# Optimization experiments

Measured on AMD Instinct MI355X. Metric: run time of the kernel, lower is better.

Reference implementation:

```python
import jax, jax.numpy as jnp
import numpy as np

B, N, F_IN = 16, 2048, 64   # batch, node_num, input_dim
D = 64                      # dim == embed_dim == GNN out_channel
TOPK = 30
EPS = 1e-5
NEG_SLOPE = 0.2


def setup_inputs() -> dict:
    key = jax.random.key(0)
    k = jax.random.split(key, 20)
    u = lambda kk, shp, b: jax.random.uniform(kk, shp, jnp.float32, -b, b)
    return {
        "data": jax.random.normal(k[0], (B, N, F_IN), jnp.float32),
        "org_edge_index": jax.random.randint(k[1], (2, N * TOPK), 0, N),  # accepted but unused (prior_graph=True)
        "embedding_weight": u(k[2], (N, D), 1.0 / np.sqrt(D)),            # kaiming_uniform(a=sqrt(5)) bound
        "lin_w": u(k[3], (F_IN, D), 1.0 / np.sqrt(F_IN)),
        "att_i": jax.random.normal(k[4], (D,), jnp.float32) * 0.1,
        "att_j": jax.random.normal(k[5], (D,), jnp.float32) * 0.1,
        "att_em_i": jax.random.normal(k[6], (D,), jnp.float32) * 0.1,
        "att_em_j": jax.random.normal(k[7], (D,), jnp.float32) * 0.1,
        "gnn_bias": jax.random.normal(k[8], (D,), jnp.float32) * 0.01,
        "bn1_gamma": jax.random.uniform(k[9], (D,), jnp.float32, 0.5, 1.5),
        "bn1_beta": jax.random.normal(k[10], (D,), jnp.float32) * 0.1,
        "bn1_mean": jax.random.normal(k[11], (D,), jnp.float32) * 0.1,
        "bn1_var": jax.random.uniform(k[12], (D,), jnp.float32, 0.5, 1.5),
        "bn2_gamma": jax.random.uniform(k[13], (D,), jnp.float32, 0.5, 1.5),
        "bn2_beta": jax.random.normal(k[14], (D,), jnp.float32) * 0.1,
        "bn2_mean": jax.random.normal(k[15], (D,), jnp.float32) * 0.1,
        "bn2_var": jax.random.uniform(k[16], (D,), jnp.float32, 0.5, 1.5),
        "out_w": u(k[17], (D, 1), 1.0 / np.sqrt(D)),
        "out_b": jnp.zeros((1,), jnp.float32),
    }


def _forward(data, org_edge_index, embedding_weight, lin_w, att_i, att_j,
             att_em_i, att_em_j, gnn_bias,
             bn1_gamma, bn1_beta, bn1_mean, bn1_var,
             bn2_gamma, bn2_beta, bn2_mean, bn2_var,
             out_w, out_b):
    b, n, f = data.shape
    x = jax.lax.stop_gradient(data).reshape(b * n, f)  # torch: x = data.clone().detach()

    # --- dynamic graph: top-k cosine similarity over DETACHED embeddings ---
    w = jax.lax.stop_gradient(embedding_weight)        # weights_arr = embedding.detach().clone()
    nrm = jnp.linalg.norm(w, axis=-1, keepdims=True)
    cos = (w @ w.T) / (nrm * nrm.T)                    # [N, N]
    _, topk_idx = jax.lax.top_k(cos, TOPK)             # [N, k]; row i contains i itself (cos(i,i)=1 is the max),
                                                       # so remove_self_loops + add_self_loops leaves the edge set unchanged
    # batched sources; target of edge (i, kk) is node i -> each node receives exactly TOPK edges
    src = (topk_idx[None] + (jnp.arange(b) * n)[:, None, None]).reshape(b * n, TOPK)

    # --- GraphLayer (GAT-style, heads=1, concat=False -> mean over 1 head) ---
    xl = x @ lin_w                                     # [BN, D]
    emb_all = jnp.tile(embedding_weight, (b, 1))       # [BN, D] embeddings repeated per batch
    a_i = xl @ att_i + emb_all @ att_em_i              # per-node target score [BN]
    a_j = xl @ att_j + emb_all @ att_em_j              # per-node source score [BN]
    alpha = jax.nn.leaky_relu(a_i[:, None] + a_j[src], NEG_SLOPE)  # [BN, k]
    alpha = jax.nn.softmax(alpha, axis=-1)             # softmax over incoming edges per target node
    out = jnp.einsum('ek,ekd->ed', alpha, xl[src]) + gnn_bias      # per-edge gather + weighted add-aggregate

    # GNNLayer: BatchNorm1d (eval) + ReLU
    out = (out - bn1_mean) / jnp.sqrt(bn1_var + EPS) * bn1_gamma + bn1_beta
    out = jax.nn.relu(out)

    # --- readout ---
    h = out.reshape(b, n, D) * embedding_weight[None]  # elementwise mul with node embeddings
    h = (h - bn2_mean) / jnp.sqrt(bn2_var + EPS) * bn2_gamma + bn2_beta  # bn_outlayer_in (eval)
    h = jax.nn.relu(h)                                 # dropout = identity (eval)
    y = h @ out_w + out_b                              # OutLayer: single Linear(D, 1)
    return y.reshape(-1, n)                            # [B, N]


def reference(data, org_edge_index, embedding_weight, lin_w, att_i, att_j,
              att_em_i, att_em_j, gnn_bias,
              bn1_gamma, bn1_beta, bn1_mean, bn1_var,
              bn2_gamma, bn2_beta, bn2_mean, bn2_var,
              out_w, out_b):
    return _forward(data, org_edge_index, embedding_weight, lin_w, att_i, att_j,
                    att_em_i, att_em_j, gnn_bias,
                    bn1_gamma, bn1_beta, bn1_mean, bn1_var,
                    bn2_gamma, bn2_beta, bn2_mean, bn2_var,
                    out_w, out_b)
```

## Files before the change

### kernel.cpp

```cpp
#include <hip/hip_runtime.h>
#include <hip/hip_bf16.h>

#define NODES 2048
#define DIM   64
#define K_TOP 30
#define BATCH 16
#define BN    (NODES * BATCH)
#define NEGINF (-3.402823466e38f)
#define EPS 1e-5f
#define TB 64

template <int CTRL>
__device__ __forceinline__ float dpp_add_f32(float x) {
    int y = __builtin_amdgcn_update_dpp(0, __float_as_int(x), CTRL, 0xf, 0xf, true);
    return x + __int_as_float(y);
}

__device__ __forceinline__ float wave_sum(float x) {
    x = dpp_add_f32<0x111>(x);
    x = dpp_add_f32<0x112>(x);
    x = dpp_add_f32<0x114>(x);
    x = dpp_add_f32<0x118>(x);
    x = dpp_add_f32<0x142>(x);
    x = dpp_add_f32<0x143>(x);
    return __int_as_float(__builtin_amdgcn_readlane(__float_as_int(x), 63));
}

template <int CTRL>
__device__ __forceinline__ float dpp_max_f32(float x) {
    int y = __builtin_amdgcn_update_dpp(__float_as_int(x), __float_as_int(x),
                                        CTRL, 0xf, 0xf, false);
    return fmaxf(x, __int_as_float(y));
}

__device__ __forceinline__ float wave_max(float x) {
    x = dpp_max_f32<0x111>(x);
    x = dpp_max_f32<0x112>(x);
    x = dpp_max_f32<0x114>(x);
    x = dpp_max_f32<0x118>(x);
    x = dpp_max_f32<0x142>(x);
    x = dpp_max_f32<0x143>(x);
    return __int_as_float(__builtin_amdgcn_readlane(__float_as_int(x), 63));
}

#define ARGMAX_STEP(CTRL)                                                       \
    do {                                                                        \
        int nv_ = __builtin_amdgcn_update_dpp(__float_as_int(bv),               \
                      __float_as_int(bv), (CTRL), 0xf, 0xf, false);             \
        int nj_ = __builtin_amdgcn_update_dpp(bj, bj, (CTRL), 0xf, 0xf, false); \
        float nvf_ = __int_as_float(nv_);                                       \
        bool g_ = (nvf_ > bv) || (nvf_ == bv && nj_ < bj);                      \
        bv = g_ ? nvf_ : bv;                                                    \
        bj = g_ ? nj_ : bj;                                                     \
    } while (0)

__global__ __launch_bounds__(256) void normalize_kernel(const float* __restrict__ w,
                                                        float* __restrict__ wn) {
    int r = blockIdx.x * 4 + (threadIdx.x >> 6);
    int lane = threadIdx.x & 63;
    float v = w[r * DIM + lane];
    float s = wave_sum(v * v);
    wn[r * DIM + lane] = v * rsqrtf(s);
}

__global__ __launch_bounds__(256) void cos_kernel(const float* __restrict__ wn,
                                                  float* __restrict__ cosm) {
    __shared__ float As[TB][DIM + 1];
    __shared__ float Bs[TB][DIM + 1];
    const int tid = threadIdx.x;
    const int bi = blockIdx.x, bj = blockIdx.y;

    for (int s = tid; s < TB * DIM; s += 256) {
        int r = s >> 6, d = s & 63;
        As[r][d] = wn[(bi * TB + r) * DIM + d];
        Bs[r][d] = wn[(bj * TB + r) * DIM + d];
    }
    __syncthreads();

    const int ti = tid >> 4, tj = tid & 15;
    float acc[4][4] = {};
    #pragma unroll 16
    for (int k = 0; k < DIM; ++k) {
        float a[4], b[4];
        #pragma unroll
        for (int u = 0; u < 4; ++u) a[u] = As[ti * 4 + u][k];
        #pragma unroll
        for (int v = 0; v < 4; ++v) b[v] = Bs[tj * 4 + v][k];
        #pragma unroll
        for (int u = 0; u < 4; ++u)
            #pragma unroll
            for (int v = 0; v < 4; ++v)
                acc[u][v] = fmaf(a[u], b[v], acc[u][v]);
    }
    #pragma unroll
    for (int u = 0; u < 4; ++u) {
        float4 o = make_float4(acc[u][0], acc[u][1], acc[u][2], acc[u][3]);
        *(float4*)&cosm[(size_t)(bi * TB + ti * 4 + u) * NODES + bj * TB + tj * 4] = o;
    }
}

__global__ __launch_bounds__(256) void topk_kernel(const float* __restrict__ cosm,
                                                   int* __restrict__ topk) {
    const int i = blockIdx.x * 4 + (threadIdx.x >> 6);
    const int lane = threadIdx.x & 63;
    const float* row = cosm + (size_t)i * NODES;

    float v[NODES / 64];
    #pragma unroll
    for (int q = 0; q < NODES / 64; ++q) v[q] = row[q * 64 + lane];

    int res = 0;
    for (int t = 0; t < K_TOP; ++t) {
        float lm = v[0];
        int lq = 0;
        #pragma unroll
        for (int q = 1; q < NODES / 64; ++q) {
            bool g = v[q] > lm;
            lm = g ? v[q] : lm;
            lq = g ? q : lq;
        }
        float bv = lm;
        int bj = lq * 64 + lane;
        ARGMAX_STEP(0x111);
        ARGMAX_STEP(0x112);
        ARGMAX_STEP(0x114);
        ARGMAX_STEP(0x118);
        ARGMAX_STEP(0x142);
        ARGMAX_STEP(0x143);
        const int wj = __builtin_amdgcn_readlane(bj, 63);
        res = (lane == t) ? wj : res;
        const int wl = wj & 63;
        const int wq = wj >> 6;
        #pragma unroll
        for (int q = 0; q < NODES / 64; ++q)
            if (q == wq && lane == wl) v[q] = NEGINF;
    }
    if (lane < K_TOP) topk[i * K_TOP + lane] = res;
}

__global__ __launch_bounds__(256) void lin_kernel(const float* __restrict__ x,
                                                  const float* __restrict__ lin_w,
                                                  const float* __restrict__ emb,
                                                  const float* __restrict__ att_i,
                                                  const float* __restrict__ att_j,
                                                  const float* __restrict__ att_em_i,
                                                  const float* __restrict__ att_em_j,
                                                  float* __restrict__ xl,
                                                  float* __restrict__ ai,
                                                  float* __restrict__ aj) {
    __shared__ float lw[DIM * DIM];
    __shared__ float xs[16 * DIM];
    const int tid = threadIdx.x;
    const int wave = tid >> 6;
    const int lane = tid & 63;
    const int row0 = blockIdx.x * 16;

    for (int t = tid; t < DIM * DIM; t += 256) lw[t] = lin_w[t];
    for (int t = tid; t < 16 * DIM; t += 256) xs[t] = x[row0 * DIM + t];
    __syncthreads();

    for (int rr = wave; rr < 16; rr += 4) {
        const int r = row0 + rr;
        float acc = 0.f;
        #pragma unroll
        for (int f = 0; f < DIM; ++f)
            acc = fmaf(xs[rr * DIM + f], lw[f * DIM + lane], acc);
        xl[r * DIM + lane] = acc;

        const int i = r & (NODES - 1);
        const float em = emb[i * DIM + lane];
        float ti = wave_sum(acc * att_i[lane] + em * att_em_i[lane]);
        float tj = wave_sum(acc * att_j[lane] + em * att_em_j[lane]);
        if (lane == 0) { ai[r] = ti; aj[r] = tj; }
    }
}

__global__ __launch_bounds__(256) void agg_kernel(const int* __restrict__ topk,
                                                  const float* __restrict__ xl,
                                                  const float* __restrict__ ai,
                                                  const float* __restrict__ aj,
                                                  const float* __restrict__ emb,
                                                  const float* __restrict__ gnn_bias,
                                                  const float* __restrict__ g1, const float* __restrict__ b1,
                                                  const float* __restrict__ m1, const float* __restrict__ v1,
                                                  const float* __restrict__ g2, const float* __restrict__ b2,
                                                  const float* __restrict__ m2, const float* __restrict__ v2,
                                                  const float* __restrict__ out_w,
                                                  const float* __restrict__ out_b,
                                                  float* __restrict__ y) {
    const int e = blockIdx.x * 4 + (threadIdx.x >> 6);
    const int lane = threadIdx.x & 63;
    const int i = e & (NODES - 1);
    const int b = e >> 11;

    const float a_ie = ai[e];
    int nbr = 0;
    float raw = NEGINF;
    if (lane < K_TOP) {
        nbr = (b << 11) + topk[i * K_TOP + lane];
        float r0 = a_ie + aj[nbr];
        raw = (r0 >= 0.f) ? r0 : 0.2f * r0;
    }
    const float m = wave_max(raw);
    float p = (lane < K_TOP) ? __expf(raw - m) : 0.f;
    const float s = wave_sum(p);
    const float inv = 1.f / s;

    float acc = 0.f;
    #pragma unroll
    for (int k = 0; k < K_TOP; ++k) {
        const float pk = __int_as_float(__builtin_amdgcn_readlane(__float_as_int(p), k));
        const int nb = __builtin_amdgcn_readlane(nbr, k);
        acc = fmaf(pk, xl[nb * DIM + lane], acc);
    }

    float o = acc * inv + gnn_bias[lane];
    o = (o - m1[lane]) * rsqrtf(v1[lane] + EPS) * g1[lane] + b1[lane];
    o = fmaxf(o, 0.f);
    float h = o * emb[i * DIM + lane];
    h = (h - m2[lane]) * rsqrtf(v2[lane] + EPS) * g2[lane] + b2[lane];
    h = fmaxf(h, 0.f);
    float t = wave_sum(h * out_w[lane]);
    if (lane == 0) y[e] = t + out_b[0];
}

extern "C" void kernel_launch(void* const* d_in, const int* in_sizes, int n_in,
                              void* d_out, int out_size, void* d_ws, size_t ws_size,
                              hipStream_t stream) {
    const float* data      = (const float*)d_in[0];
    const float* emb       = (const float*)d_in[2];
    const float* lin_w     = (const float*)d_in[3];
    const float* att_i     = (const float*)d_in[4];
    const float* att_j     = (const float*)d_in[5];
    const float* att_em_i  = (const float*)d_in[6];
    const float* att_em_j  = (const float*)d_in[7];
    const float* gnn_bias  = (const float*)d_in[8];
    const float* bn1_gamma = (const float*)d_in[9];
    const float* bn1_beta  = (const float*)d_in[10];
    const float* bn1_mean  = (const float*)d_in[11];
    const float* bn1_var   = (const float*)d_in[12];
    const float* bn2_gamma = (const float*)d_in[13];
    const float* bn2_beta  = (const float*)d_in[14];
    const float* bn2_mean  = (const float*)d_in[15];
    const float* bn2_var   = (const float*)d_in[16];
    const float* out_w     = (const float*)d_in[17];
    const float* out_b     = (const float*)d_in[18];
    float* y = (float*)d_out;

    char* ws = (char*)d_ws;
    float* cosm = (float*)(ws);
    float* xl   = (float*)(ws);
    float* ai   = (float*)(ws + 8 * 1024 * 1024);
    float* aj   = (float*)(ws + 8 * 1024 * 1024 + 131072);
    float* wn   = (float*)(ws + 16 * 1024 * 1024);
    int*   topk = (int*)  (ws + 16 * 1024 * 1024 + 524288);

    normalize_kernel<<<NODES / 4, 256, 0, stream>>>(emb, wn);
    cos_kernel<<<dim3(NODES / TB, NODES / TB), 256, 0, stream>>>(wn, cosm);
    topk_kernel<<<NODES / 4, 256, 0, stream>>>(cosm, topk);
    lin_kernel<<<BN / 16, 256, 0, stream>>>(data, lin_w, emb, att_i, att_j,
                                            att_em_i, att_em_j, xl, ai, aj);
    agg_kernel<<<BN / 4, 256, 0, stream>>>(topk, xl, ai, aj, emb, gnn_bias,
                                           bn1_gamma, bn1_beta, bn1_mean, bn1_var,
                                           bn2_gamma, bn2_beta, bn2_mean, bn2_var,
                                           out_w, out_b, y);
}
```

Baseline: 178.8 us.

## Retile cosine GEMM with transposed LDS and tree-reduce per-lane top-k argmax

The cosine-similarity kernel moves to 128x128 tiles with 512 threads, an 8x4 register tile per thread, and embeddings stored transposed in shared memory so each step reads operands as float4. This is meant to raise compute per shared-memory load and cut load instruction count, at the cost of more registers and possible bank conflicts on the transposed stores. The top-k kernel replaces the serial 32-element per-lane argmax chain with a pairwise tree reduction, which shortens the dependency chain in each of the 30 selection rounds. The tree keeps the lower index on ties, so results stay the same.

```diff
diff --git a/kernel.cpp b/kernel.cpp
--- a/kernel.cpp
+++ b/kernel.cpp
@@ -8,7 +8,8 @@
 #define BN    (NODES * BATCH)
 #define NEGINF (-3.402823466e38f)
 #define EPS 1e-5f
-#define TB 64
+#define TBC 128
+#define KPAD 132
 
 template <int CTRL>
 __device__ __forceinline__ float dpp_add_f32(float x) {
@@ -63,39 +64,42 @@
     wn[r * DIM + lane] = v * rsqrtf(s);
 }
 
-__global__ __launch_bounds__(256) void cos_kernel(const float* __restrict__ wn,
+__global__ __launch_bounds__(512) void cos_kernel(const float* __restrict__ wn,
                                                   float* __restrict__ cosm) {
-    __shared__ float As[TB][DIM + 1];
-    __shared__ float Bs[TB][DIM + 1];
+    __shared__ float AsT[DIM][KPAD];
+    __shared__ float BsT[DIM][KPAD];
     const int tid = threadIdx.x;
     const int bi = blockIdx.x, bj = blockIdx.y;
 
-    for (int s = tid; s < TB * DIM; s += 256) {
+    #pragma unroll
+    for (int it = 0; it < 16; ++it) {
+        int s = it * 512 + tid;
         int r = s >> 6, d = s & 63;
-        As[r][d] = wn[(bi * TB + r) * DIM + d];
-        Bs[r][d] = wn[(bj * TB + r) * DIM + d];
+        AsT[d][r] = wn[(bi * TBC + r) * DIM + d];
+        BsT[d][r] = wn[(bj * TBC + r) * DIM + d];
     }
     __syncthreads();
 
-    const int ti = tid >> 4, tj = tid & 15;
-    float acc[4][4] = {};
-    #pragma unroll 16
+    const int ti = tid >> 5;
+    const int tj = tid & 31;
+    float acc[8][4] = {};
+    #pragma unroll 4
     for (int k = 0; k < DIM; ++k) {
-        float a[4], b[4];
-        #pragma unroll
-        for (int u = 0; u < 4; ++u) a[u] = As[ti * 4 + u][k];
-        #pragma unroll
-        for (int v = 0; v < 4; ++v) b[v] = Bs[tj * 4 + v][k];
-        #pragma unroll
-        for (int u = 0; u < 4; ++u)
+        float4 a0 = *(const float4*)&AsT[k][ti * 8];
+        float4 a1 = *(const float4*)&AsT[k][ti * 8 + 4];
+        float4 b0 = *(const float4*)&BsT[k][tj * 4];
+        float a[8] = {a0.x, a0.y, a0.z, a0.w, a1.x, a1.y, a1.z, a1.w};
+        float b[4] = {b0.x, b0.y, b0.z, b0.w};
+        #pragma unroll
+        for (int u = 0; u < 8; ++u)
             #pragma unroll
             for (int v = 0; v < 4; ++v)
                 acc[u][v] = fmaf(a[u], b[v], acc[u][v]);
     }
     #pragma unroll
-    for (int u = 0; u < 4; ++u) {
+    for (int u = 0; u < 8; ++u) {
         float4 o = make_float4(acc[u][0], acc[u][1], acc[u][2], acc[u][3]);
-        *(float4*)&cosm[(size_t)(bi * TB + ti * 4 + u) * NODES + bj * TB + tj * 4] = o;
+        *(float4*)&cosm[(size_t)(bi * TBC + ti * 8 + u) * NODES + bj * TBC + tj * 4] = o;
     }
 }
 
@@ -111,16 +115,24 @@
 
     int res = 0;
     for (int t = 0; t < K_TOP; ++t) {
-        float lm = v[0];
-        int lq = 0;
-        #pragma unroll
-        for (int q = 1; q < NODES / 64; ++q) {
-            bool g = v[q] > lm;
-            lm = g ? v[q] : lm;
-            lq = g ? q : lq;
+        float tv[16]; int tq[16];
+        #pragma unroll
+        for (int u = 0; u < 16; ++u) {
+            bool g = v[2 * u + 1] > v[2 * u];
+            tv[u] = g ? v[2 * u + 1] : v[2 * u];
+            tq[u] = g ? (2 * u + 1) : (2 * u);
         }
-        float bv = lm;
-        int bj = lq * 64 + lane;
+        #pragma unroll
+        for (int h = 8; h >= 1; h >>= 1) {
+            #pragma unroll
+            for (int u = 0; u < h; ++u) {
+                bool g = tv[u + h] > tv[u];
+                tv[u] = g ? tv[u + h] : tv[u];
+                tq[u] = g ? tq[u + h] : tq[u];
+            }
+        }
+        float bv = tv[0];
+        int bj = tq[0] * 64 + lane;
         ARGMAX_STEP(0x111);
         ARGMAX_STEP(0x112);
         ARGMAX_STEP(0x114);
@@ -256,7 +268,7 @@
     int*   topk = (int*)  (ws + 16 * 1024 * 1024 + 524288);
 
     normalize_kernel<<<NODES / 4, 256, 0, stream>>>(emb, wn);
-    cos_kernel<<<dim3(NODES / TB, NODES / TB), 256, 0, stream>>>(wn, cosm);
+    cos_kernel<<<dim3(NODES / TBC, NODES / TBC), 512, 0, stream>>>(wn, cosm);
     topk_kernel<<<NODES / 4, 256, 0, stream>>>(cosm, topk);
     lin_kernel<<<BN / 16, 256, 0, stream>>>(data, lin_w, emb, att_i, att_j,
                                             att_em_i, att_em_j, xl, ai, aj);
```

Measured after the change: 212.4 us. 1.19x slower.
